# Performance work log

Hardware: AMD Instinct MI355X
Metric: run time of the kernel (lower is better)

The kernel has to match this reference:

```python
import jax, jax.numpy as jnp
import numpy as np

SPLINE_ORDER = 3
BN_EPS = 1e-5


def make_grid(grid_size, lo=-1.0, hi=1.0):
    # torch KANLinear grid: uniform on [lo,hi] extended by spline_order knots each side
    h = (hi - lo) / grid_size
    return jnp.arange(-SPLINE_ORDER, grid_size + SPLINE_ORDER + 1, dtype=jnp.float32) * h + lo


def b_splines(x, grid, k=SPLINE_ORDER):
    # x: [...], grid: [G+2k+1] -> bases [..., G+k] (Cox-de Boor recursion)
    x = x[..., None]
    bases = ((x >= grid[:-1]) & (x < grid[1:])).astype(x.dtype)
    for j in range(1, k + 1):
        left = (x - grid[: -(j + 1)]) / (grid[j:-1] - grid[: -(j + 1)])
        right = (grid[j + 1:] - x) / (grid[j + 1:] - grid[1:-j])
        bases = left * bases[..., :-1] + right * bases[..., 1:]
    return bases


def extract_patches(x, d):
    # 3x3 dilated sliding windows, stride 1, padding == dilation -> same HxW
    B, C, H, W = x.shape
    xp = jnp.pad(x, ((0, 0), (0, 0), (d, d), (d, d)))
    pats = [xp[:, :, ki * d:ki * d + H, kj * d:kj * d + W]
            for ki in range(3) for kj in range(3)]
    return jnp.stack(pats, axis=-1)  # [B,C,H,W,9] (kh-major, matching torch Unfold)


def batchnorm(x, g, b):
    # training-mode BN (torch default forward): batch statistics, biased variance
    mean = x.mean(axis=(0, 2, 3), keepdims=True)
    var = x.var(axis=(0, 2, 3), keepdims=True)
    return (x - mean) / jnp.sqrt(var + BN_EPS) * g[None, :, None, None] + b[None, :, None, None]


def se_block(x, w1, w2):
    y = x.mean(axis=(2, 3))                                  # [B,C]
    y = jax.nn.sigmoid(jax.nn.relu(y @ w1.T) @ w2.T)         # [B,C]
    return x * y[:, :, None, None]


def kan_conv(x, base_w, spline_w, grid, dilation):
    # one KANLinear(9->1) per (out,in) channel pair, summed over in channels
    p = extract_patches(x, dilation)                          # [B,Ci,H,W,9]
    base = jnp.einsum('bihwk,oik->bohw', jax.nn.silu(p), base_w)
    bs = b_splines(p, grid)                                   # [B,Ci,H,W,9,G+k]
    spl = jnp.einsum('bihwkg,oikg->bohw', bs, spline_w)
    return base + spl


def kan_branch(x, base_w, spline_w, grid, dilation, bn_g, bn_b, se_w1, se_w2):
    y = kan_conv(x, base_w, spline_w, grid, dilation)
    y = jax.nn.relu(batchnorm(y, bn_g, bn_b))
    return se_block(y, se_w1, se_w2)


def setup_inputs() -> dict:
    key = jax.random.key(0)
    ks = jax.random.split(key, 16)
    B, Ci, Co, H, W = 2, 64, 64, 64, 64
    r = Co // 16
    d = {"x": jax.random.normal(ks[0], (B, Ci, H, W), jnp.float32)}
    for i, (bname, G) in enumerate([(6, 3), (12, 6), (18, 9)]):
        kk = jax.random.split(ks[1 + i], 4)
        d[f"base_w{bname}"] = jax.random.normal(kk[0], (Co, Ci, 9), jnp.float32) / np.sqrt(9.0 * Ci)
        d[f"spline_w{bname}"] = jax.random.normal(kk[1], (Co, Ci, 9, G + SPLINE_ORDER), jnp.float32) * (0.1 / np.sqrt(9.0 * Ci))
        d[f"bn{bname}_g"] = jnp.ones((Co,), jnp.float32)
        d[f"bn{bname}_b"] = jnp.zeros((Co,), jnp.float32)
        d[f"se{bname}_w1"] = jax.random.normal(kk[2], (r, Co), jnp.float32) / np.sqrt(Co)
        d[f"se{bname}_w2"] = jax.random.normal(kk[3], (Co, r), jnp.float32) / np.sqrt(r)
    d["gp_conv_w"] = jax.random.normal(ks[4], (Co, Ci), jnp.float32) / np.sqrt(Ci)
    d["gp_conv_b"] = jnp.zeros((Co,), jnp.float32)
    d["gp_bn_g"] = jnp.ones((Co,), jnp.float32)
    d["gp_bn_b"] = jnp.zeros((Co,), jnp.float32)
    d["gp_se_w1"] = jax.random.normal(ks[5], (r, Co), jnp.float32) / np.sqrt(Co)
    d["gp_se_w2"] = jax.random.normal(ks[6], (Co, r), jnp.float32) / np.sqrt(r)
    d["fuse_w"] = jax.random.normal(ks[7], (Co, 4 * Co), jnp.float32) / np.sqrt(4.0 * Co)
    d["fuse_b"] = jnp.zeros((Co,), jnp.float32)
    d["fuse_bn_g"] = jnp.ones((Co,), jnp.float32)
    d["fuse_bn_b"] = jnp.zeros((Co,), jnp.float32)
    return d


def reference(x, base_w6, spline_w6, bn6_g, bn6_b, se6_w1, se6_w2,
              base_w12, spline_w12, bn12_g, bn12_b, se12_w1, se12_w2,
              base_w18, spline_w18, bn18_g, bn18_b, se18_w1, se18_w2,
              gp_conv_w, gp_conv_b, gp_bn_g, gp_bn_b, gp_se_w1, gp_se_w2,
              fuse_w, fuse_b, fuse_bn_g, fuse_bn_b):
    B, Ci, H, W = x.shape
    # global-pool branch: avgpool -> 1x1 conv -> BN -> ReLU -> SE -> bilinear
    # upsample (1x1 source => pure broadcast, align_corners irrelevant)
    gp = x.mean(axis=(2, 3)) @ gp_conv_w.T + gp_conv_b      # [B,Co]
    gp = gp[:, :, None, None]
    gp = jax.nn.relu(batchnorm(gp, gp_bn_g, gp_bn_b))
    gp = se_block(gp, gp_se_w1, gp_se_w2)
    gp = jnp.broadcast_to(gp, (B, gp.shape[1], H, W))
    # KAN dilated branches
    b6 = kan_branch(x, base_w6, spline_w6, make_grid(3), 6, bn6_g, bn6_b, se6_w1, se6_w2)
    b12 = kan_branch(x, base_w12, spline_w12, make_grid(6), 12, bn12_g, bn12_b, se12_w1, se12_w2)
    b18 = kan_branch(x, base_w18, spline_w18, make_grid(9), 18, bn18_g, bn18_b, se18_w1, se18_w2)
    cat = jnp.concatenate([b6, b12, b18, gp], axis=1)        # [B,4Co,H,W]
    out = jnp.einsum('bihw,oi->bohw', cat, fuse_w) + fuse_b[None, :, None, None]
    out = jax.nn.relu(batchnorm(out, fuse_bn_g, fuse_bn_b))
    return out
```

## Files before the change

kernel.cpp:

```cpp
#include <hip/hip_runtime.h>
#include <hip/hip_bf16.h>
#include <math.h>

#define DEV __device__ __forceinline__

static constexpr int HW  = 4096;
static constexpr int POS = 8192;
static constexpr int SLAB = 6 * 64 * 4096;

typedef __attribute__((ext_vector_type(8)))  short short8;
typedef __attribute__((ext_vector_type(16))) float floatx16;

template<int G>
DEV void bsplines(float x, float* out ) {
  const float h = 2.0f / (float)G;
  float knot[G + 7];
#pragma unroll
  for (int t = 0; t < G + 7; ++t) knot[t] = -1.0f + (float)(t - 3) * h;
  float bb[G + 6];
#pragma unroll
  for (int t = 0; t < G + 6; ++t) bb[t] = (x >= knot[t] && x < knot[t + 1]) ? 1.0f : 0.0f;
#pragma unroll
  for (int j = 1; j <= 3; ++j) {
    const float inv = (float)G / (2.0f * (float)j);
#pragma unroll
    for (int t = 0; t < G + 6 - j; ++t) {
      float left  = (x - knot[t]) * inv;
      float right = (knot[t + j + 1] - x) * inv;
      bb[t] = left * bb[t] + right * bb[t + 1];
    }
  }
#pragma unroll
  for (int t = 0; t < G + 3; ++t) out[t] = bb[t];
}

DEV float sigmoidf_(float x) { return 1.0f / (1.0f + __expf(-x)); }

DEV float block_reduce_256(float v, float* sb) {
  __syncthreads();
#pragma unroll
  for (int off = 32; off > 0; off >>= 1) v += __shfl_down(v, off, 64);
  int lane = threadIdx.x & 63, wid = threadIdx.x >> 6;
  if (lane == 0) sb[wid] = v;
  __syncthreads();
  return sb[0] + sb[1] + sb[2] + sb[3];
}


template<int CF>
DEV void wprep_body(const float* __restrict__ base_w, const float* __restrict__ spline_w,
                    __hip_bfloat16* __restrict__ Wt, int bid) {
  constexpr int KC = 64 * CF;
  int lin = bid * 256 + threadIdx.x;
  int ic = lin % KC;
  int rest = lin / KC;
  int o = rest & 63, tap = rest >> 6;
  int c = ic % CF, i = ic / CF;
  float v = (c == 0) ? base_w[(o * 64 + i) * 9 + tap]
                     : spline_w[((o * 64 + i) * 9 + tap) * (CF - 1) + (c - 1)];
  Wt[lin] = __float2bfloat16(v);
}

template<int G>
DEV void c0r_body(int ki, const float* __restrict__ sw, float* __restrict__ out,
                  float* shmem ) {
  constexpr int NB = G + 3;
  int o = threadIdx.x & 63, part = threadIdx.x >> 6;
  float b0[NB];
  bsplines<G>(0.0f, b0);
  float s = 0.0f;
  for (int kj = 0; kj < 3; ++kj) {
    int tap = ki * 3 + kj;
    for (int i = part * 16; i < part * 16 + 16; ++i) {
      const float* p = sw + ((size_t)(o * 64 + i) * 9 + tap) * NB;
#pragma unroll
      for (int c = 0; c < NB; ++c) s += p[c] * b0[c];
    }
  }
  shmem[part * 64 + o] = s;
  __syncthreads();
  if (part == 0)
    out[ki * 64 + o] = shmem[o] + shmem[64 + o] + shmem[128 + o] + shmem[192 + o];
}

template<int G, int D>
DEV void features_body(const float* __restrict__ x, __hip_bfloat16* __restrict__ F, int bid,
                       __hip_bfloat16* lds ) {
  constexpr int CF = G + 4;
  constexpr int NB = G + 3;
  constexpr int WP = 64 + 2 * D;
  constexpr int NG = WP / 4;
  constexpr int KC = 64 * CF;
  int i = threadIdx.x & 63, ws = threadIdx.x >> 6;
  int wpg = bid % NG;
  int rest = bid / NG;
  int h = rest & 63, b = rest >> 6;
  int wp = wpg * 4 + ws;
  int w = wp - D;
  float xv = (w >= 0 && w < 64) ? x[((size_t)(b * 64 + i) * 64 + h) * 64 + w] : 0.0f;
  float s = xv * sigmoidf_(xv);
  float bas[NB];
  bsplines<G>(xv, bas);
  __hip_bfloat16* dst = lds + (ws * 64 + i) * CF;
  dst[0] = __float2bfloat16(s);
#pragma unroll
  for (int c = 1; c < CF; ++c) dst[c] = __float2bfloat16(bas[c - 1]);
  __syncthreads();
  constexpr int TOT2 = 4 * 64 * CF / 2;
  uint* g = (uint*)(F + ((size_t)((b * 64 + h) * WP) + wpg * 4) * KC);
  const uint* l = (const uint*)lds;
  for (int t = threadIdx.x; t < TOT2; t += 256) g[t] = l[t];
}

__global__ void prepfeat_k(const float* __restrict__ x,
                           __hip_bfloat16* F0, __hip_bfloat16* F1, __hip_bfloat16* F2,
                           const float* bw0, const float* sw0, const float* bw1,
                           const float* sw1, const float* bw2, const float* sw2,
                           __hip_bfloat16* W0, __hip_bfloat16* W1, __hip_bfloat16* W2,
                           float* C0r, const float* fuse_w, float* fwT,
                           float* xm, float* accz ) {
  __shared__ __hip_bfloat16 lds[4 * 64 * 13];
  __shared__ float shmem[256];
  int bid = blockIdx.x, tid = threadIdx.x;
  if (bid < 2432)      { features_body<3, 6>(x, F0, bid, lds); return; }
  else if (bid < 5248) { features_body<6, 12>(x, F1, bid - 2432, lds); return; }
  else if (bid < 8448) { features_body<9, 18>(x, F2, bid - 5248, lds); return; }
  int pb = bid - 8448;
  if (pb < 1008)      { wprep_body<7>(bw0, sw0, W0, pb); }
  else if (pb < 2448) { wprep_body<10>(bw1, sw1, W1, pb - 1008); }
  else if (pb < 4320) { wprep_body<13>(bw2, sw2, W2, pb - 2448); }
  else if (pb < 4329) {
    int idx = pb - 4320, br = idx / 3, ki = idx % 3;
    if (br == 0)      c0r_body<3>(ki, sw0, C0r, shmem);
    else if (br == 1) c0r_body<6>(ki, sw1, C0r + 192, shmem);
    else              c0r_body<9>(ki, sw2, C0r + 384, shmem);
  } else if (pb < 4377) {
    int lin = (pb - 4329) * 256 + tid;
    int o = lin & 63, i2 = lin >> 6;
    fwT[i2 * 64 + o] = fuse_w[o * 256 + i2];
  } else if (pb < 4505) {
    int bi = pb - 4377;
    const float* p = x + (size_t)bi * HW;
    float s = 0.0f;
    for (int t = tid; t < HW; t += 256) s += p[t];
    s = block_reduce_256(s, shmem);
    if (tid == 0) xm[bi] = s * (1.0f / HW);
  } else {
    for (int t = tid; t < 896; t += 256) accz[t] = 0.0f;
  }
}

DEV floatx16 mfma_bf16(short8 a, short8 b, floatx16 c) {
  return __builtin_amdgcn_mfma_f32_32x32x16_bf16(a, b, c, 0, 0, 0);
}

template<int CF, int DD>
DEV void conv_dev(int ki, int b, int hp, const short* __restrict__ F,
                  const short* __restrict__ W, const float* __restrict__ C0r,
                  float* __restrict__ ypart, int br) {
  constexpr int KC = 64 * CF;
  constexpr int WP = 64 + 2 * DD;
  int wv = threadIdx.x >> 6;
  int lane = threadIdx.x & 63;
  int lr = lane & 31, lq = lane >> 5;
  int hs = hp * 2 + wv;
  int h_out = hs - (ki - 1) * DD;
  bool valid = (h_out >= 0 && h_out < 64);
  int h_tgt = valid ? h_out : (h_out < 0 ? h_out + 64 : h_out - 64);
  float* yb = ypart + (size_t)ki * SLAB + ((size_t)((br * 2 + b) * 64 + h_tgt)) * 4096;

  if (!valid) {
    const float* c0 = C0r + (br * 3 + ki) * 64;
#pragma unroll
    for (int wh = 0; wh < 2; ++wh) {
      int w = wh * 32 + lr;
#pragma unroll
      for (int ot = 0; ot < 2; ++ot)
#pragma unroll
        for (int reg = 0; reg < 16; ++reg) {
          int o = (reg & 3) + 8 * (reg >> 2) + 4 * lq + 32 * ot;
          yb[(size_t)o * 64 + w] = c0[o];
        }
    }
    return;
  }

  floatx16 acc[2][2];
#pragma unroll
  for (int ot = 0; ot < 2; ++ot)
#pragma unroll
    for (int wh = 0; wh < 2; ++wh)
#pragma unroll
      for (int r = 0; r < 16; ++r) acc[ot][wh][r] = 0.0f;

  const short* rowF = F + (size_t)(b * 64 + hs) * WP * KC;
  const short* wb = W + (size_t)(ki * 3) * 64 * KC + lr * KC + lq * 8;
  const short* fb = rowF + lr * KC + lq * 8;
#pragma unroll
  for (int kj = 0; kj < 3; ++kj) {
    const short* w0p = wb + kj * (64 * KC);
    const short* f0p = fb + kj * (DD * KC);
#pragma unroll 4
    for (int s = 0; s < 4 * CF; ++s) {
      short8 a0 = *(const short8*)(w0p + s * 16);
      short8 a1 = *(const short8*)(w0p + 32 * KC + s * 16);
      short8 b0 = *(const short8*)(f0p + s * 16);
      short8 b1 = *(const short8*)(f0p + 32 * KC + s * 16);
      acc[0][0] = mfma_bf16(a0, b0, acc[0][0]);
      acc[0][1] = mfma_bf16(a0, b1, acc[0][1]);
      acc[1][0] = mfma_bf16(a1, b0, acc[1][0]);
      acc[1][1] = mfma_bf16(a1, b1, acc[1][1]);
    }
  }

#pragma unroll
  for (int ot = 0; ot < 2; ++ot)
#pragma unroll
    for (int wh = 0; wh < 2; ++wh) {
      int w = wh * 32 + lr;
#pragma unroll
      for (int reg = 0; reg < 16; ++reg) {
        int o = (reg & 3) + 8 * (reg >> 2) + 4 * lq + 32 * ot;
        yb[(size_t)o * 64 + w] = acc[ot][wh][reg];
      }
    }
}

__global__ __launch_bounds__(128) void conv_all_k(
    const short* __restrict__ F0, const short* __restrict__ F1, const short* __restrict__ F2,
    const short* __restrict__ W0, const short* __restrict__ W1, const short* __restrict__ W2,
    const float* __restrict__ C0r, float* __restrict__ ypart) {
  int bid = blockIdx.x;
  int e  = bid & 7;
  int t  = bid >> 3;
  int ki = t % 3;
  int m  = (t / 3) * 8 + e;
  int br = m >> 6, b = (m >> 5) & 1, hp = m & 31;
  if (br == 0)      conv_dev<7, 6>(ki, b, hp, F0, W0, C0r, ypart, 0);
  else if (br == 1) conv_dev<10, 12>(ki, b, hp, F1, W1, C0r, ypart, 1);
  else              conv_dev<13, 18>(ki, b, hp, F2, W2, C0r, ypart, 2);
}

__global__ void rb_k(float* __restrict__ yp, float* __restrict__ bnacc_s,
                     float* __restrict__ bnacc_q) {
  int bid = blockIdx.x;
  int bb = bid / 256, chunk = bid % 256;
  int br = bb >> 1;
  int tid = threadIdx.x;
  size_t base = (size_t)bb * 262144 + chunk * 1024 + tid * 4;
  float4 v = *(const float4*)(yp + base);
#pragma unroll
  for (int s2 = 1; s2 < 3; ++s2) {
    float4 u = *(const float4*)(yp + base + (size_t)s2 * SLAB);
    v.x += u.x; v.y += u.y; v.z += u.z; v.w += u.w;
  }
  *(float4*)(yp + base) = v;
  float s = v.x + v.y + v.z + v.w;
  float q = v.x * v.x + v.y * v.y + v.z * v.z + v.w * v.w;
  s += __shfl_down(s, 8, 16); s += __shfl_down(s, 4, 16);
  s += __shfl_down(s, 2, 16); s += __shfl_down(s, 1, 16);
  q += __shfl_down(q, 8, 16); q += __shfl_down(q, 4, 16);
  q += __shfl_down(q, 2, 16); q += __shfl_down(q, 1, 16);
  if ((tid & 15) == 0) {
    int o = (chunk * 16 + (tid >> 4)) & 63;
    atomicAdd(&bnacc_s[br * 64 + o], s);
    atomicAdd(&bnacc_q[br * 64 + o], q);
  }
}

__global__ void sesum_k(const float* __restrict__ y, const float* __restrict__ bnacc_s,
                        const float* __restrict__ bnacc_q,
                        const float* g0, const float* b0p, const float* g1, const float* b1p,
                        const float* g2, const float* b2p, float* __restrict__ se_acc) {
  int bid = blockIdx.x;
  int bb = bid >> 6, h = bid & 63;
  int br = bb >> 1;
  int tid = threadIdx.x;
  int o = tid >> 2, wq = tid & 3;
  const float* gptr = (br == 0) ? g0 : ((br == 1) ? g1 : g2);
  const float* bptr = (br == 0) ? b0p : ((br == 1) ? b1p : b2p);
  float mu = bnacc_s[br * 64 + o] * (1.0f / POS);
  float var = bnacc_q[br * 64 + o] * (1.0f / POS) - mu * mu;
  float kk = gptr[o] / sqrtf(var + 1e-5f);
  float cc = bptr[o] - mu * kk;
  const float* row = y + (size_t)bb * 262144 + (size_t)h * 4096 + o * 64 + wq * 16;
  float s = 0.0f;
#pragma unroll
  for (int j = 0; j < 4; ++j) {
    float4 v = *(const float4*)(row + j * 4);
    float a;
    a = v.x * kk + cc; s += (a > 0.0f) ? a : 0.0f;
    a = v.y * kk + cc; s += (a > 0.0f) ? a : 0.0f;
    a = v.z * kk + cc; s += (a > 0.0f) ? a : 0.0f;
    a = v.w * kk + cc; s += (a > 0.0f) ? a : 0.0f;
  }
  s += __shfl_down(s, 2, 4);
  s += __shfl_down(s, 1, 4);
  if (wq == 0) atomicAdd(&se_acc[bb * 64 + o], s);
}

__global__ void semlp_gp_k(const float* __restrict__ se_acc,
                           const float* __restrict__ bnacc_s, const float* __restrict__ bnacc_q,
                           const float* g0, const float* b0p, const float* g1, const float* b1p,
                           const float* g2, const float* b2p,
                           const float* w10, const float* w11, const float* w12,
                           const float* w20, const float* w21, const float* w22,
                           float* __restrict__ A1, float* __restrict__ A0,
                           const float* __restrict__ xm, const float* __restrict__ gw,
                           const float* __restrict__ gb, const float* __restrict__ bng,
                           const float* __restrict__ bnb, const float* __restrict__ gpw1,
                           const float* __restrict__ gpw2, const float* __restrict__ fuse_w,
                           float* __restrict__ fuse_gp) {
  __shared__ float sm[64];
  __shared__ float g0s[2][64], gp1s[2][64], gpvs[2][64];
  int tid = threadIdx.x;
  if (blockIdx.x < 6) {
    int bb = blockIdx.x, br = bb >> 1;
    const float* w1 = (br == 0) ? w10 : ((br == 1) ? w11 : w12);
    const float* w2 = (br == 0) ? w20 : ((br == 1) ? w21 : w22);
    const float* gptr = (br == 0) ? g0 : ((br == 1) ? g1 : g2);
    const float* bptr = (br == 0) ? b0p : ((br == 1) ? b1p : b2p);
    if (tid < 64) sm[tid] = se_acc[bb * 64 + tid] * (1.0f / HW);
    __syncthreads();
    if (tid < 64) {
      int o = tid;
      float z[4];
#pragma unroll
      for (int j = 0; j < 4; ++j) {
        float s = 0.0f;
        for (int c2 = 0; c2 < 64; ++c2) s += sm[c2] * w1[j * 64 + c2];
        z[j] = (s > 0.0f) ? s : 0.0f;
      }
      float t = 0.0f;
#pragma unroll
      for (int j = 0; j < 4; ++j) t += z[j] * w2[o * 4 + j];
      t = sigmoidf_(t);
      float mu = bnacc_s[br * 64 + o] * (1.0f / POS);
      float var = bnacc_q[br * 64 + o] * (1.0f / POS) - mu * mu;
      float kk = gptr[o] / sqrtf(var + 1e-5f);
      float cc = bptr[o] - mu * kk;
      A1[bb * 64 + o] = kk * t;
      A0[bb * 64 + o] = cc * t;
    }
  } else {
    int b = tid >> 6, o = tid & 63;
    float gv = gb[o];
    for (int i = 0; i < 64; ++i) gv += xm[b * 64 + i] * gw[o * 64 + i];
    g0s[b][o] = gv;
    __syncthreads();
    float mu = 0.5f * (g0s[0][o] + g0s[1][o]);
    float df = g0s[0][o] - g0s[1][o];
    float var = 0.25f * df * df;
    float v = (gv - mu) / sqrtf(var + 1e-5f) * bng[o] + bnb[o];
    v = (v > 0.0f) ? v : 0.0f;
    gp1s[b][o] = v;
    __syncthreads();
    float z[4];
#pragma unroll
    for (int j = 0; j < 4; ++j) {
      float s = 0.0f;
      for (int c2 = 0; c2 < 64; ++c2) s += gp1s[b][c2] * gpw1[j * 64 + c2];
      z[j] = (s > 0.0f) ? s : 0.0f;
    }
    float t = 0.0f;
#pragma unroll
    for (int j = 0; j < 4; ++j) t += z[j] * gpw2[o * 4 + j];
    t = sigmoidf_(t);
    gpvs[b][o] = v * t;
    __syncthreads();
    float fg = 0.0f;
    for (int c2 = 0; c2 < 64; ++c2) fg += fuse_w[o * 256 + 192 + c2] * gpvs[b][c2];
    fuse_gp[b * 64 + o] = fg;
  }
}

__global__ __launch_bounds__(256) void fuse_k(
    const float* __restrict__ y, const float* __restrict__ A1, const float* __restrict__ A0,
    const float* __restrict__ fwT, const float* __restrict__ fb, const float* __restrict__ fgp,
    float* __restrict__ tmp, float* __restrict__ fstat) {
  int bid = blockIdx.x;
  int b = bid >> 7, h = (bid >> 1) & 63, wh = bid & 1;
  int tid = threadIdx.x;
  int wg = tid & 7, og = tid >> 3;
  int w0 = wg * 4, o0 = og * 2;
  float acc[2][4] = {};
  __shared__ float As[64][32];
  __shared__ float Ws[64][64];
  for (int br = 0; br < 3; ++br) {
#pragma unroll
    for (int m = 0; m < 8; ++m) {
      int lin = tid + m * 256;
      int oc = lin >> 5, wl = lin & 31;
      float v = y[(size_t)(br * 2 + b) * 262144 + (size_t)h * 4096 + oc * 64 + wh * 32 + wl];
      float a1 = A1[(br * 2 + b) * 64 + oc], a0 = A0[(br * 2 + b) * 64 + oc];
      v = v * a1 + a0;
      As[oc][wl] = (v > 0.0f) ? v : 0.0f;
    }
#pragma unroll
    for (int m = 0; m < 16; ++m) {
      int lin = tid + m * 256;
      int oc = lin >> 6, ol = lin & 63;
      Ws[oc][ol] = fwT[(br * 64 + oc) * 64 + ol];
    }
    __syncthreads();
#pragma unroll 8
    for (int ict = 0; ict < 64; ++ict) {
      float4 a = *reinterpret_cast<const float4*>(&As[ict][w0]);
      float2 wv = *reinterpret_cast<const float2*>(&Ws[ict][o0]);
      acc[0][0] += wv.x * a.x; acc[0][1] += wv.x * a.y; acc[0][2] += wv.x * a.z; acc[0][3] += wv.x * a.w;
      acc[1][0] += wv.y * a.x; acc[1][1] += wv.y * a.y; acc[1][2] += wv.y * a.z; acc[1][3] += wv.y * a.w;
    }
    __syncthreads();
  }
  float* tp = tmp + (size_t)(b * 64 + h) * 4096 + wh * 32;
  float ps[2], pq[2];
#pragma unroll
  for (int oo = 0; oo < 2; ++oo) {
    int o = o0 + oo;
    float bias = fb[o] + fgp[b * 64 + o];
    float4 v = make_float4(acc[oo][0] + bias, acc[oo][1] + bias,
                           acc[oo][2] + bias, acc[oo][3] + bias);
    *reinterpret_cast<float4*>(&tp[o * 64 + w0]) = v;
    ps[oo] = v.x + v.y + v.z + v.w;
    pq[oo] = v.x * v.x + v.y * v.y + v.z * v.z + v.w * v.w;
  }
  __syncthreads();
#pragma unroll
  for (int oo = 0; oo < 2; ++oo) { As[o0 + oo][wg] = ps[oo]; Ws[o0 + oo][wg] = pq[oo]; }
  __syncthreads();
  if (tid < 64) {
    float s = 0.0f, q = 0.0f;
#pragma unroll
    for (int r = 0; r < 8; ++r) { s += As[tid][r]; q += Ws[tid][r]; }
    atomicAdd(&fstat[tid], s);
    atomicAdd(&fstat[64 + tid], q);
  }
}

__global__ void final_k(const float* __restrict__ tmp, const float* __restrict__ fstat,
                        const float* __restrict__ g, const float* __restrict__ bb,
                        float* __restrict__ out) {
  int lin = blockIdx.x * 256 + threadIdx.x;
  int w = lin & 63, h2 = (lin >> 6) & 63, o = (lin >> 12) & 63, b = lin >> 18;
  float v = tmp[((size_t)(b * 64 + h2) * 64 + o) * 64 + w];
  float m = fstat[o] * (1.0f / POS);
  float var = fstat[64 + o] * (1.0f / POS) - m * m;
  float kk = g[o] / sqrtf(var + 1e-5f);
  float r = (v - m) * kk + bb[o];
  out[lin] = (r > 0.0f) ? r : 0.0f;
}

extern "C" void kernel_launch(void* const* d_in, const int* in_sizes, int n_in,
                              void* d_out, int out_size, void* d_ws, size_t ws_size,
                              hipStream_t stream) {
  const float* x = (const float*)d_in[0];
  const float* base_w[3]   = {(const float*)d_in[1],  (const float*)d_in[7],  (const float*)d_in[13]};
  const float* spline_w[3] = {(const float*)d_in[2],  (const float*)d_in[8],  (const float*)d_in[14]};
  const float* bn_g[3]     = {(const float*)d_in[3],  (const float*)d_in[9],  (const float*)d_in[15]};
  const float* bn_b[3]     = {(const float*)d_in[4],  (const float*)d_in[10], (const float*)d_in[16]};
  const float* se_w1[3]    = {(const float*)d_in[5],  (const float*)d_in[11], (const float*)d_in[17]};
  const float* se_w2[3]    = {(const float*)d_in[6],  (const float*)d_in[12], (const float*)d_in[18]};
  const float* gp_conv_w = (const float*)d_in[19];
  const float* gp_conv_b = (const float*)d_in[20];
  const float* gp_bn_g   = (const float*)d_in[21];
  const float* gp_bn_b   = (const float*)d_in[22];
  const float* gp_se_w1  = (const float*)d_in[23];
  const float* gp_se_w2  = (const float*)d_in[24];
  const float* fuse_w    = (const float*)d_in[25];
  const float* fuse_b    = (const float*)d_in[26];
  const float* fuse_bn_g = (const float*)d_in[27];
  const float* fuse_bn_b = (const float*)d_in[28];
  float* out = (float*)d_out;

  char* wsp = (char*)d_ws;
  auto alloc = [&](size_t bytes) -> char* {
    char* p = wsp;
    wsp += (bytes + 255) & ~(size_t)255;
    return p;
  };
  __hip_bfloat16* F0 = (__hip_bfloat16*)alloc((size_t)2 * 64 * 76 * 448 * 2);
  __hip_bfloat16* F1 = (__hip_bfloat16*)alloc((size_t)2 * 64 * 88 * 640 * 2);
  __hip_bfloat16* F2 = (__hip_bfloat16*)alloc((size_t)2 * 64 * 100 * 832 * 2);
  __hip_bfloat16* W0 = (__hip_bfloat16*)alloc((size_t)9 * 64 * 448 * 2);
  __hip_bfloat16* W1 = (__hip_bfloat16*)alloc((size_t)9 * 64 * 640 * 2);
  __hip_bfloat16* W2 = (__hip_bfloat16*)alloc((size_t)9 * 64 * 832 * 2);
  float* C0r   = (float*)alloc((size_t)3 * 3 * 64 * 4);
  float* ypart = (float*)alloc((size_t)3 * SLAB * 4);
  float* y     = ypart;
  float* tmp   = ypart + SLAB;
  float* A1  = (float*)alloc(384 * 4);
  float* A0  = (float*)alloc(384 * 4);
  float* xm  = (float*)alloc(128 * 4);
  float* fgp = (float*)alloc(128 * 4);
  float* fwT = (float*)alloc((size_t)12288 * 4);
  float* accz = (float*)alloc(896 * 4);
  float* fstat   = accz;
  float* bnacc_s = accz + 128;
  float* bnacc_q = accz + 320;
  float* se_acc  = accz + 512;

  prepfeat_k<<<12954, 256, 0, stream>>>(x, F0, F1, F2,
                                        base_w[0], spline_w[0], base_w[1], spline_w[1],
                                        base_w[2], spline_w[2], W0, W1, W2, C0r,
                                        fuse_w, fwT, xm, accz);
  conv_all_k<<<576, 128, 0, stream>>>(
      (const short*)F0, (const short*)F1, (const short*)F2,
      (const short*)W0, (const short*)W1, (const short*)W2, C0r, ypart);
  rb_k<<<1536, 256, 0, stream>>>(ypart, bnacc_s, bnacc_q);
  sesum_k<<<384, 256, 0, stream>>>(y, bnacc_s, bnacc_q, bn_g[0], bn_b[0], bn_g[1], bn_b[1],
                                   bn_g[2], bn_b[2], se_acc);
  semlp_gp_k<<<7, 128, 0, stream>>>(se_acc, bnacc_s, bnacc_q, bn_g[0], bn_b[0], bn_g[1], bn_b[1],
                                    bn_g[2], bn_b[2], se_w1[0], se_w1[1], se_w1[2],
                                    se_w2[0], se_w2[1], se_w2[2], A1, A0,
                                    xm, gp_conv_w, gp_conv_b, gp_bn_g, gp_bn_b,
                                    gp_se_w1, gp_se_w2, fuse_w, fgp);
  fuse_k<<<256, 256, 0, stream>>>(y, A1, A0, fwT, fuse_b, fgp, tmp, fstat);
  final_k<<<2048, 256, 0, stream>>>(tmp, fstat, fuse_bn_g, fuse_bn_b, out);
}
```

Before: 291.2 us.

## Split conv kj taps across three waves with LDS reduction

The conv kernel now launches three times as many waves per block. Each wave pair handles one of the three kj taps, so the serial K loop per wave shrinks threefold. Partial accumulators from kj=1 and kj=2 are summed through a padded LDS buffer with two block barriers, and the kj=0 waves write the final sum. This is meant to raise parallelism on the MFMA-bound conv with only 576 small blocks. The cost is about 33KB of LDS per block and extra synchronisation.

```diff
diff --git a/kernel.cpp b/kernel.cpp
--- a/kernel.cpp
+++ b/kernel.cpp
@@ -157,10 +157,12 @@
 template<int CF, int DD>
 DEV void conv_dev(int ki, int b, int hp, const short* __restrict__ F,
                   const short* __restrict__ W, const float* __restrict__ C0r,
-                  float* __restrict__ ypart, int br) {
+                  float* __restrict__ ypart, int br, float* __restrict__ red) {
   constexpr int KC = 64 * CF;
   constexpr int WP = 64 + 2 * DD;
-  int wv = threadIdx.x >> 6;
+  int wid = threadIdx.x >> 6;
+  int wv  = wid & 1;
+  int kjw = wid >> 1;
   int lane = threadIdx.x & 63;
   int lr = lane & 31, lq = lane >> 5;
   int hs = hp * 2 + wv;
@@ -169,22 +171,6 @@
   int h_tgt = valid ? h_out : (h_out < 0 ? h_out + 64 : h_out - 64);
   float* yb = ypart + (size_t)ki * SLAB + ((size_t)((br * 2 + b) * 64 + h_tgt)) * 4096;
 
-  if (!valid) {
-    const float* c0 = C0r + (br * 3 + ki) * 64;
-#pragma unroll
-    for (int wh = 0; wh < 2; ++wh) {
-      int w = wh * 32 + lr;
-#pragma unroll
-      for (int ot = 0; ot < 2; ++ot)
-#pragma unroll
-        for (int reg = 0; reg < 16; ++reg) {
-          int o = (reg & 3) + 8 * (reg >> 2) + 4 * lq + 32 * ot;
-          yb[(size_t)o * 64 + w] = c0[o];
-        }
-    }
-    return;
-  }
-
   floatx16 acc[2][2];
 #pragma unroll
   for (int ot = 0; ot < 2; ++ot)
@@ -193,13 +179,10 @@
 #pragma unroll
       for (int r = 0; r < 16; ++r) acc[ot][wh][r] = 0.0f;
 
-  const short* rowF = F + (size_t)(b * 64 + hs) * WP * KC;
-  const short* wb = W + (size_t)(ki * 3) * 64 * KC + lr * KC + lq * 8;
-  const short* fb = rowF + lr * KC + lq * 8;
-#pragma unroll
-  for (int kj = 0; kj < 3; ++kj) {
-    const short* w0p = wb + kj * (64 * KC);
-    const short* f0p = fb + kj * (DD * KC);
+  if (valid) {
+    const short* rowF = F + (size_t)(b * 64 + hs) * WP * KC;
+    const short* w0p = W + (size_t)(ki * 3 + kjw) * 64 * KC + lr * KC + lq * 8;
+    const short* f0p = rowF + (size_t)kjw * (DD * KC) + lr * KC + lq * 8;
 #pragma unroll 4
     for (int s = 0; s < 4 * CF; ++s) {
       short8 a0 = *(const short8*)(w0p + s * 16);
@@ -213,32 +196,73 @@
     }
   }
 
-#pragma unroll
-  for (int ot = 0; ot < 2; ++ot)
+  float* slot = red + (size_t)wv * (64 * 65) + lane * 65;
+  if (kjw == 2 && valid) {
+#pragma unroll
+    for (int ot = 0; ot < 2; ++ot)
+#pragma unroll
+      for (int wh = 0; wh < 2; ++wh)
+#pragma unroll
+        for (int r = 0; r < 16; ++r) slot[(ot * 2 + wh) * 16 + r] = acc[ot][wh][r];
+  }
+  __syncthreads();
+  if (kjw == 1 && valid) {
+#pragma unroll
+    for (int ot = 0; ot < 2; ++ot)
+#pragma unroll
+      for (int wh = 0; wh < 2; ++wh)
+#pragma unroll
+        for (int r = 0; r < 16; ++r) {
+          int idx = (ot * 2 + wh) * 16 + r;
+          slot[idx] += acc[ot][wh][r];
+        }
+  }
+  __syncthreads();
+  if (kjw != 0) return;
+
+  if (!valid) {
+    const float* c0 = C0r + (br * 3 + ki) * 64;
 #pragma unroll
     for (int wh = 0; wh < 2; ++wh) {
       int w = wh * 32 + lr;
 #pragma unroll
-      for (int reg = 0; reg < 16; ++reg) {
-        int o = (reg & 3) + 8 * (reg >> 2) + 4 * lq + 32 * ot;
-        yb[(size_t)o * 64 + w] = acc[ot][wh][reg];
+      for (int ot = 0; ot < 2; ++ot)
+#pragma unroll
+        for (int r = 0; r < 16; ++r) {
+          int o = (r & 3) + 8 * (r >> 2) + 4 * lq + 32 * ot;
+          yb[(size_t)o * 64 + w] = c0[o];
+        }
+    }
+    return;
+  }
+
+#pragma unroll
+  for (int ot = 0; ot < 2; ++ot)
+#pragma unroll
+    for (int wh = 0; wh < 2; ++wh) {
+      int w = wh * 32 + lr;
+#pragma unroll
+      for (int r = 0; r < 16; ++r) {
+        int o = (r & 3) + 8 * (r >> 2) + 4 * lq + 32 * ot;
+        yb[(size_t)o * 64 + w] = acc[ot][wh][r] + slot[(ot * 2 + wh) * 16 + r];
       }
     }
 }
 
-__global__ __launch_bounds__(128) void conv_all_k(
+__global__ __launch_bounds__(384) void conv_all_k(
     const short* __restrict__ F0, const short* __restrict__ F1, const short* __restrict__ F2,
     const short* __restrict__ W0, const short* __restrict__ W1, const short* __restrict__ W2,
     const float* __restrict__ C0r, float* __restrict__ ypart) {
+  __shared__ float red[2 * 64 * 65];
   int bid = blockIdx.x;
   int e  = bid & 7;
   int t  = bid >> 3;
   int ki = t % 3;
   int m  = (t / 3) * 8 + e;
   int br = m >> 6, b = (m >> 5) & 1, hp = m & 31;
-  if (br == 0)      conv_dev<7, 6>(ki, b, hp, F0, W0, C0r, ypart, 0);
-  else if (br == 1) conv_dev<10, 12>(ki, b, hp, F1, W1, C0r, ypart, 1);
-  else              conv_dev<13, 18>(ki, b, hp, F2, W2, C0r, ypart, 2);
+  if (br == 0)      conv_dev<7, 6>(ki, b, hp, F0, W0, C0r, ypart, 0, red);
+  else if (br == 1) conv_dev<10, 12>(ki, b, hp, F1, W1, C0r, ypart, 1, red);
+  else              conv_dev<13, 18>(ki, b, hp, F2, W2, C0r, ypart, 2, red);
 }
 
 __global__ void rb_k(float* __restrict__ yp, float* __restrict__ bnacc_s,
@@ -503,7 +527,7 @@
                                         base_w[0], spline_w[0], base_w[1], spline_w[1],
                                         base_w[2], spline_w[2], W0, W1, W2, C0r,
                                         fuse_w, fwT, xm, accz);
-  conv_all_k<<<576, 128, 0, stream>>>(
+  conv_all_k<<<576, 384, 0, stream>>>(
       (const short*)F0, (const short*)F1, (const short*)F2,
       (const short*)W0, (const short*)W1, (const short*)W2, C0r, ypart);
   rb_k<<<1536, 256, 0, stream>>>(ypart, bnacc_s, bnacc_q);
```

Measured after the change: 297.2 us. 2.1% more time.
